# Performance work log

Hardware: AMD Instinct MI355X
Metric: run time of the kernel (lower is better)

The kernel has to match this reference:

```python
import jax, jax.numpy as jnp
import numpy as np

TEMPERATURE = 0.1
EPS = 1e-8


def setup_inputs() -> dict:
    key = jax.random.key(0)
    k1, k2 = jax.random.split(key)
    N, D = 4096, 512
    features = jax.random.normal(k1, (N, D), dtype=jnp.float32)
    labels = jax.random.randint(k2, (N,), 0, 100, dtype=jnp.int64)
    return {"features": features, "labels": labels}


def reference(features, labels):
    # FFT along feature dim -> complex (N, D)
    cf = jnp.fft.fft(features)
    N = cf.shape[0]

    # All-pairs complex dot product expressed as a GEMM:
    # Re(sum_d u_d * conj(v_d)) for every (anchor, contrast) pair -> (N, N)
    dot_real = jnp.real(cf @ jnp.conj(cf).T)

    # L2 norm of complex vectors: sqrt(sum |cf|^2) -> (N,)
    norms = jnp.linalg.norm(cf, axis=-1)

    sim = dot_real / (norms[:, None] * norms[None, :])  # cosine sim (N, N)
    sim = sim / TEMPERATURE

    # Positive-pair mask (same label), excluding the diagonal (self)
    same_label = (labels[:, None] == labels[None, :]).astype(sim.dtype)
    logits_mask = 1.0 - jnp.eye(N, dtype=sim.dtype)
    mask = same_label * logits_mask

    # Faithful to the original: exp without max-subtraction (sim bounded by 1/tau)
    exp_logits = jnp.exp(sim) * logits_mask
    log_prob = sim - jnp.log(exp_logits.sum(axis=1, keepdims=True))

    mean_log_prob_pos = (mask * log_prob).sum(axis=1) / (mask.sum(axis=1) + EPS)
    return -mean_log_prob_pos.mean()
```

## Files before the change

### kernel.cpp

```cpp
#include <hip/hip_runtime.h>
#include <hip/hip_bf16.h>
#include <math.h>


#define NROWS 4096
#define DDIM  512
#define BAND  128
#define NBAND (NROWS / BAND)
#define NPAIR (NBAND * (NBAND + 1) / 2)
#define NSTEP 16

typedef __attribute__((ext_vector_type(4))) float floatx4;

__device__ inline long f8pack(float v0, float v1, float v2, float v3,
                              float v4, float v5, float v6, float v7) {
    int lo = 0, hi = 0;
    lo = __builtin_amdgcn_cvt_pk_fp8_f32(v0, v1, lo, false);
    lo = __builtin_amdgcn_cvt_pk_fp8_f32(v2, v3, lo, true);
    hi = __builtin_amdgcn_cvt_pk_fp8_f32(v4, v5, hi, false);
    hi = __builtin_amdgcn_cvt_pk_fp8_f32(v6, v7, hi, true);
    return ((long)(unsigned)lo) | ((long)hi << 32);
}

__device__ inline float dpp_add16(float v) {
    v += __int_as_float(__builtin_amdgcn_update_dpp(
        0, __float_as_int(v), 0xB1, 0xF, 0xF, true));
    v += __int_as_float(__builtin_amdgcn_update_dpp(
        0, __float_as_int(v), 0x4E, 0xF, 0xF, true));
    v += __int_as_float(__builtin_amdgcn_update_dpp(
        0, __float_as_int(v), 0x141, 0xF, 0xF, true));
    v += __int_as_float(__builtin_amdgcn_update_dpp(
        0, __float_as_int(v), 0x140, 0xF, 0xF, true));
    return v;
}

__global__ __launch_bounds__(256) void prep_kernel(
    const float* __restrict__ F, const int* __restrict__ labels,
    long* __restrict__ Fq, float* __restrict__ invn,
    float* __restrict__ S, float* __restrict__ P, int* __restrict__ hist) {
    const int g = blockIdx.x, t = threadIdx.x;
    const int l = t & 63, w = t >> 6;
    const int row = g * 16 + (l & 15);
    const int koff = ((l >> 4) & 3) * 8;
    float ss = 0.f;
#pragma unroll
    for (int c = 0; c < 4; ++c) {
        const int s = c * 4 + w;
        const int k = s * 32 + koff;
        const float4* src = (const float4*)(F + (size_t)row * DDIM + k);
        float4 a = src[0], b = src[1];
        ss += a.x * a.x + a.y * a.y + a.z * a.z + a.w * a.w
            + b.x * b.x + b.y * b.y + b.z * b.z + b.w * b.w;
        Fq[(size_t)(g * 16 + s) * 64 + l] =
            f8pack(a.x, a.y, a.z, a.w, b.x, b.y, b.z, b.w);
    }
    ss += __shfl_xor(ss, 16, 64);
    ss += __shfl_xor(ss, 32, 64);
    __shared__ float rs[4][16];
    if (l < 16) rs[w][l] = ss;
    __syncthreads();
    if (t < 16) {
        float tot = rs[0][t] + rs[1][t] + rs[2][t] + rs[3][t];
        int r = g * 16 + t;
        invn[r] = rsqrtf(tot) * 3.16227766017f;
        S[r] = 0.f;
        P[r] = 0.f;
    }
    if (g == 0) {
        __shared__ int h[128];
        if (t < 128) h[t] = 0;
        __syncthreads();
        for (int i = t; i < NROWS; i += 256) atomicAdd(&h[labels[i]], 1);
        __syncthreads();
        if (t < 128) hist[t] = h[t];
    }
}

__global__ __launch_bounds__(256) void gemm_kernel(
    const long* __restrict__ Fq, const float* __restrict__ invn,
    const int* __restrict__ labels,
    float* __restrict__ S, float* __restrict__ P) {
    __shared__ long Asl[BAND * 64];

    const int tid = threadIdx.x;
    const int w = tid >> 6, lane = tid & 63;
    const int lrow = lane & 15, lquad = lane >> 4;

    int wid = blockIdx.x;
    int bi = 0;
    while ((bi + 1) * NBAND - (bi + 1) * bi / 2 <= wid) ++bi;
    const int bj = bi + (wid - (bi * NBAND - bi * (bi - 1) / 2));
    const bool diag = (bi == bj);
    const int ib = bi * BAND, jb = bj * BAND;

    {
        const long* src = Fq + (size_t)bi * 8192;
#pragma unroll
        for (int r = 0; r < 16; ++r) {
            __builtin_amdgcn_global_load_lds(
                (const __attribute__((address_space(1))) unsigned int*)
                    (src + r * 512 + (size_t)tid * 2),
                (__attribute__((address_space(3))) unsigned int*)
                    (Asl + r * 512 + tid * 2),
                16, 0, 0);
        }
    }
    __syncthreads();

    floatx4 acc[8][2];
#pragma unroll
    for (int mi = 0; mi < 8; ++mi) {
        acc[mi][0] = (floatx4){0.f, 0.f, 0.f, 0.f};
        acc[mi][1] = (floatx4){0.f, 0.f, 0.f, 0.f};
    }

    const long* pB0 = Fq + (size_t)(bj * 8 + w * 2) * 1024 + lane;
    const long* pB1 = Fq + (size_t)(bj * 8 + w * 2 + 1) * 1024 + lane;

    long bring[2][2];
    bring[0][0] = pB0[0];
    bring[0][1] = pB1[0];
    bring[1][0] = pB0[64];
    bring[1][1] = pB1[64];

#pragma unroll
    for (int ks = 0; ks < NSTEP; ++ks) {
        const int cur = ks & 1;
        const long b0 = bring[cur][0], b1 = bring[cur][1];
        if (ks + 2 < NSTEP) {
            bring[cur][0] = pB0[(ks + 2) * 64];
            bring[cur][1] = pB1[(ks + 2) * 64];
        }
        long a[8];
#pragma unroll
        for (int mi = 0; mi < 8; ++mi)
            a[mi] = Asl[(mi * 16 + ks) * 64 + lane];
#pragma unroll
        for (int mi = 0; mi < 8; ++mi) {
            acc[mi][0] = __builtin_amdgcn_mfma_f32_16x16x32_fp8_fp8(
                a[mi], b0, acc[mi][0], 0, 0, 0);
            acc[mi][1] = __builtin_amdgcn_mfma_f32_16x16x32_fp8_fp8(
                a[mi], b1, acc[mi][1], 0, 0, 0);
        }
    }

    __syncthreads();
    float* er = (float*)Asl;
    float* pr = er + 128;
    float* ec = pr + 128;
    float* pc = ec + 128;
    ((float*)Asl)[tid] = 0.f;
    ((float*)Asl)[tid + 256] = 0.f;
    __syncthreads();

    float inB[2];
    int lB[2];
#pragma unroll
    for (int ni = 0; ni < 2; ++ni) {
        int j = jb + (w * 2 + ni) * 16 + lrow;
        inB[ni] = invn[j];
        lB[ni] = labels[j];
    }

    float ecol[2] = {0.f, 0.f}, pcol[2] = {0.f, 0.f};
#pragma unroll
    for (int mi = 0; mi < 8; ++mi) {
#pragma unroll
        for (int r = 0; r < 4; ++r) {
            const int il = mi * 16 + lquad * 4 + r;
            const int i = ib + il;
            const float inA = invn[i];
            const int lA = labels[i];
            float es = 0.f, ps = 0.f;
#pragma unroll
            for (int ni = 0; ni < 2; ++ni) {
                const int j = jb + (w * 2 + ni) * 16 + lrow;
                float sim = acc[mi][ni][r] * inA * inB[ni];
                float e = __expf(sim);
                float pm = (lA == lB[ni]) ? sim : 0.f;
                if (diag && i == j) { e = 0.f; pm = 0.f; }
                es += e; ps += pm;
                ecol[ni] += e; pcol[ni] += pm;
            }
            es = dpp_add16(es);
            ps = dpp_add16(ps);
            if (lrow == 0) {
                atomicAdd(&er[il], es);
                atomicAdd(&pr[il], ps);
            }
        }
    }
#pragma unroll
    for (int ni = 0; ni < 2; ++ni) {
        float e = ecol[ni], p = pcol[ni];
        e += __shfl_xor(e, 16, 64);
        e += __shfl_xor(e, 32, 64);
        p += __shfl_xor(p, 16, 64);
        p += __shfl_xor(p, 32, 64);
        if (lquad == 0) {
            atomicAdd(&ec[(w * 2 + ni) * 16 + lrow], e);
            atomicAdd(&pc[(w * 2 + ni) * 16 + lrow], p);
        }
    }
    __syncthreads();
    if (tid < 128) {
        atomicAdd(&S[ib + tid], er[tid]);
        atomicAdd(&P[ib + tid], pr[tid]);
    } else if (!diag) {
        atomicAdd(&S[jb + tid - 128], ec[tid - 128]);
        atomicAdd(&P[jb + tid - 128], pc[tid - 128]);
    }
}

__global__ __launch_bounds__(256) void final_kernel(
    const float* __restrict__ S, const float* __restrict__ P,
    const int* __restrict__ labels, const int* __restrict__ hist,
    float* __restrict__ out) {
    float local = 0.f;
    for (int i = threadIdx.x; i < NROWS; i += 256) {
        float cnt = (float)(hist[labels[i]] - 1);
        local += (P[i] - cnt * logf(S[i])) / (cnt + 1e-8f);
    }
#pragma unroll
    for (int m = 1; m < 64; m <<= 1) local += __shfl_xor(local, m, 64);
    __shared__ float red[4];
    int wave = threadIdx.x >> 6;
    if ((threadIdx.x & 63) == 0) red[wave] = local;
    __syncthreads();
    if (threadIdx.x == 0)
        out[0] = -(red[0] + red[1] + red[2] + red[3]) / (float)NROWS;
}

extern "C" void kernel_launch(void* const* d_in, const int* in_sizes, int n_in,
                              void* d_out, int out_size, void* d_ws, size_t ws_size,
                              hipStream_t stream) {
    const float* F = (const float*)d_in[0];
    const int* labels = (const int*)d_in[1];
    float* out = (float*)d_out;

    long* Fq = (long*)d_ws;
    float* invn = (float*)((char*)d_ws + (size_t)NROWS * DDIM);
    float* S = invn + NROWS;
    float* P = S + NROWS;
    int* hist = (int*)(P + NROWS);

    prep_kernel<<<dim3(NROWS / 16), dim3(256), 0, stream>>>(
        F, labels, Fq, invn, S, P, hist);
    gemm_kernel<<<dim3(NPAIR), dim3(256), 0, stream>>>(
        Fq, invn, labels, S, P);
    final_kernel<<<dim3(1), dim3(256), 0, stream>>>(S, P, labels, hist, out);
}
```

Baseline: 95.06 us.

## Fuse prep, GEMM and final reduction into one persistent kernel with grid barriers

Replaces the three separate kernels with a single persistent kernel of 264 workgroups. A spin-wait global barrier on atomic counters separates the quantize/norm phase, the tiled FP8 MFMA pass (each workgroup takes two of the 528 band pairs) and the final reduction done by workgroup 0. The aim is to remove kernel launch gaps and tail effects. It also deepens the B-operand register prefetch from two stages to three. The grid barrier depends on all 264 workgroups being co-resident, and it adds a small init kernel plus spin overhead.

```diff
diff --git a/kernel.cpp b/kernel.cpp
--- a/kernel.cpp
+++ b/kernel.cpp
@@ -8,6 +8,7 @@
 #define BAND  128
 #define NBAND (NROWS / BAND)
 #define NPAIR (NBAND * (NBAND + 1) / 2)
+#define NWG   264
 #define NSTEP 16
 
 typedef __attribute__((ext_vector_type(4))) float floatx4;
@@ -34,201 +35,218 @@
     return v;
 }
 
-__global__ __launch_bounds__(256) void prep_kernel(
+__global__ __launch_bounds__(64) void init_bar(int* __restrict__ bar) {
+    if (threadIdx.x < 8) bar[threadIdx.x] = 0;
+}
+
+__device__ inline void gbar(int* __restrict__ bar, int slot) {
+    __syncthreads();
+    if (threadIdx.x == 0) {
+        __threadfence();
+        atomicAdd(&bar[slot], 1);
+        while (__hip_atomic_load(&bar[slot], __ATOMIC_RELAXED,
+                                 __HIP_MEMORY_SCOPE_AGENT) < NWG)
+            __builtin_amdgcn_s_sleep(2);
+        __threadfence();
+    }
+    __syncthreads();
+}
+
+__global__ __launch_bounds__(256, 2) void fused_all(
     const float* __restrict__ F, const int* __restrict__ labels,
     long* __restrict__ Fq, float* __restrict__ invn,
-    float* __restrict__ S, float* __restrict__ P, int* __restrict__ hist) {
-    const int g = blockIdx.x, t = threadIdx.x;
-    const int l = t & 63, w = t >> 6;
-    const int row = g * 16 + (l & 15);
-    const int koff = ((l >> 4) & 3) * 8;
-    float ss = 0.f;
-#pragma unroll
-    for (int c = 0; c < 4; ++c) {
-        const int s = c * 4 + w;
-        const int k = s * 32 + koff;
-        const float4* src = (const float4*)(F + (size_t)row * DDIM + k);
-        float4 a = src[0], b = src[1];
-        ss += a.x * a.x + a.y * a.y + a.z * a.z + a.w * a.w
-            + b.x * b.x + b.y * b.y + b.z * b.z + b.w * b.w;
-        Fq[(size_t)(g * 16 + s) * 64 + l] =
-            f8pack(a.x, a.y, a.z, a.w, b.x, b.y, b.z, b.w);
-    }
-    ss += __shfl_xor(ss, 16, 64);
-    ss += __shfl_xor(ss, 32, 64);
-    __shared__ float rs[4][16];
-    if (l < 16) rs[w][l] = ss;
-    __syncthreads();
-    if (t < 16) {
-        float tot = rs[0][t] + rs[1][t] + rs[2][t] + rs[3][t];
-        int r = g * 16 + t;
-        invn[r] = rsqrtf(tot) * 3.16227766017f;
-        S[r] = 0.f;
-        P[r] = 0.f;
-    }
-    if (g == 0) {
-        __shared__ int h[128];
-        if (t < 128) h[t] = 0;
-        __syncthreads();
-        for (int i = t; i < NROWS; i += 256) atomicAdd(&h[labels[i]], 1);
-        __syncthreads();
-        if (t < 128) hist[t] = h[t];
-    }
-}
-
-__global__ __launch_bounds__(256) void gemm_kernel(
-    const long* __restrict__ Fq, const float* __restrict__ invn,
-    const int* __restrict__ labels,
-    float* __restrict__ S, float* __restrict__ P) {
+    float* __restrict__ S, float* __restrict__ P,
+    int* __restrict__ hist, int* __restrict__ bar,
+    float* __restrict__ out) {
     __shared__ long Asl[BAND * 64];
-
+    const int wg = blockIdx.x;
     const int tid = threadIdx.x;
     const int w = tid >> 6, lane = tid & 63;
     const int lrow = lane & 15, lquad = lane >> 4;
 
-    int wid = blockIdx.x;
-    int bi = 0;
-    while ((bi + 1) * NBAND - (bi + 1) * bi / 2 <= wid) ++bi;
-    const int bj = bi + (wid - (bi * NBAND - bi * (bi - 1) / 2));
-    const bool diag = (bi == bj);
-    const int ib = bi * BAND, jb = bj * BAND;
-
-    {
-        const long* src = Fq + (size_t)bi * 8192;
-#pragma unroll
-        for (int r = 0; r < 16; ++r) {
-            __builtin_amdgcn_global_load_lds(
-                (const __attribute__((address_space(1))) unsigned int*)
-                    (src + r * 512 + (size_t)tid * 2),
-                (__attribute__((address_space(3))) unsigned int*)
-                    (Asl + r * 512 + tid * 2),
-                16, 0, 0);
-        }
-    }
-    __syncthreads();
-
-    floatx4 acc[8][2];
-#pragma unroll
-    for (int mi = 0; mi < 8; ++mi) {
-        acc[mi][0] = (floatx4){0.f, 0.f, 0.f, 0.f};
-        acc[mi][1] = (floatx4){0.f, 0.f, 0.f, 0.f};
-    }
-
-    const long* pB0 = Fq + (size_t)(bj * 8 + w * 2) * 1024 + lane;
-    const long* pB1 = Fq + (size_t)(bj * 8 + w * 2 + 1) * 1024 + lane;
-
-    long bring[2][2];
-    bring[0][0] = pB0[0];
-    bring[0][1] = pB1[0];
-    bring[1][0] = pB0[64];
-    bring[1][1] = pB1[64];
-
-#pragma unroll
-    for (int ks = 0; ks < NSTEP; ++ks) {
-        const int cur = ks & 1;
-        const long b0 = bring[cur][0], b1 = bring[cur][1];
-        if (ks + 2 < NSTEP) {
-            bring[cur][0] = pB0[(ks + 2) * 64];
-            bring[cur][1] = pB1[(ks + 2) * 64];
-        }
-        long a[8];
-#pragma unroll
-        for (int mi = 0; mi < 8; ++mi)
-            a[mi] = Asl[(mi * 16 + ks) * 64 + lane];
+    if (wg < NROWS / 16) {
+        const int g = wg;
+        const int row = g * 16 + (lane & 15);
+        const int koff = ((lane >> 4) & 3) * 8;
+        float ss = 0.f;
+#pragma unroll
+        for (int c = 0; c < 4; ++c) {
+            const int s = c * 4 + w;
+            const int k = s * 32 + koff;
+            const float4* src = (const float4*)(F + (size_t)row * DDIM + k);
+            float4 a = src[0], b = src[1];
+            ss += a.x * a.x + a.y * a.y + a.z * a.z + a.w * a.w
+                + b.x * b.x + b.y * b.y + b.z * b.z + b.w * b.w;
+            Fq[(size_t)(g * 16 + s) * 64 + lane] =
+                f8pack(a.x, a.y, a.z, a.w, b.x, b.y, b.z, b.w);
+        }
+        ss += __shfl_xor(ss, 16, 64);
+        ss += __shfl_xor(ss, 32, 64);
+        float* rs = (float*)Asl;
+        if (lane < 16) rs[w * 16 + lane] = ss;
+        __syncthreads();
+        if (tid < 16) {
+            float tot = rs[tid] + rs[16 + tid] + rs[32 + tid] + rs[48 + tid];
+            int r = g * 16 + tid;
+            invn[r] = rsqrtf(tot) * 3.16227766017f;
+            S[r] = 0.f;
+            P[r] = 0.f;
+        }
+        if (g == 0) {
+            int* h = (int*)Asl + 64;
+            __syncthreads();
+            if (tid < 128) h[tid] = 0;
+            __syncthreads();
+            for (int i = tid; i < NROWS; i += 256) atomicAdd(&h[labels[i]], 1);
+            __syncthreads();
+            if (tid < 128) hist[tid] = h[tid];
+        }
+    }
+    gbar(bar, 0);
+
+#pragma unroll 1
+    for (int rep = 0; rep < 2; ++rep) {
+        const int wid = wg + rep * NWG;
+        int bi = 0;
+        while ((bi + 1) * NBAND - (bi + 1) * bi / 2 <= wid) ++bi;
+        const int bj = bi + (wid - (bi * NBAND - bi * (bi - 1) / 2));
+        const bool diag = (bi == bj);
+        const int ib = bi * BAND, jb = bj * BAND;
+
+        __syncthreads();
+        {
+            const long* src = Fq + (size_t)bi * 8192;
+#pragma unroll
+            for (int r = 0; r < 16; ++r) {
+                __builtin_amdgcn_global_load_lds(
+                    (const __attribute__((address_space(1))) unsigned int*)
+                        (src + r * 512 + (size_t)tid * 2),
+                    (__attribute__((address_space(3))) unsigned int*)
+                        (Asl + r * 512 + tid * 2),
+                    16, 0, 0);
+            }
+        }
+        __syncthreads();
+
+        floatx4 acc[8][2];
 #pragma unroll
         for (int mi = 0; mi < 8; ++mi) {
-            acc[mi][0] = __builtin_amdgcn_mfma_f32_16x16x32_fp8_fp8(
-                a[mi], b0, acc[mi][0], 0, 0, 0);
-            acc[mi][1] = __builtin_amdgcn_mfma_f32_16x16x32_fp8_fp8(
-                a[mi], b1, acc[mi][1], 0, 0, 0);
-        }
-    }
-
-    __syncthreads();
-    float* er = (float*)Asl;
-    float* pr = er + 128;
-    float* ec = pr + 128;
-    float* pc = ec + 128;
-    ((float*)Asl)[tid] = 0.f;
-    ((float*)Asl)[tid + 256] = 0.f;
-    __syncthreads();
-
-    float inB[2];
-    int lB[2];
-#pragma unroll
-    for (int ni = 0; ni < 2; ++ni) {
-        int j = jb + (w * 2 + ni) * 16 + lrow;
-        inB[ni] = invn[j];
-        lB[ni] = labels[j];
-    }
-
-    float ecol[2] = {0.f, 0.f}, pcol[2] = {0.f, 0.f};
-#pragma unroll
-    for (int mi = 0; mi < 8; ++mi) {
-#pragma unroll
-        for (int r = 0; r < 4; ++r) {
-            const int il = mi * 16 + lquad * 4 + r;
-            const int i = ib + il;
-            const float inA = invn[i];
-            const int lA = labels[i];
-            float es = 0.f, ps = 0.f;
-#pragma unroll
-            for (int ni = 0; ni < 2; ++ni) {
-                const int j = jb + (w * 2 + ni) * 16 + lrow;
-                float sim = acc[mi][ni][r] * inA * inB[ni];
-                float e = __expf(sim);
-                float pm = (lA == lB[ni]) ? sim : 0.f;
-                if (diag && i == j) { e = 0.f; pm = 0.f; }
-                es += e; ps += pm;
-                ecol[ni] += e; pcol[ni] += pm;
-            }
-            es = dpp_add16(es);
-            ps = dpp_add16(ps);
-            if (lrow == 0) {
-                atomicAdd(&er[il], es);
-                atomicAdd(&pr[il], ps);
-            }
-        }
-    }
-#pragma unroll
-    for (int ni = 0; ni < 2; ++ni) {
-        float e = ecol[ni], p = pcol[ni];
-        e += __shfl_xor(e, 16, 64);
-        e += __shfl_xor(e, 32, 64);
-        p += __shfl_xor(p, 16, 64);
-        p += __shfl_xor(p, 32, 64);
-        if (lquad == 0) {
-            atomicAdd(&ec[(w * 2 + ni) * 16 + lrow], e);
-            atomicAdd(&pc[(w * 2 + ni) * 16 + lrow], p);
-        }
-    }
-    __syncthreads();
-    if (tid < 128) {
-        atomicAdd(&S[ib + tid], er[tid]);
-        atomicAdd(&P[ib + tid], pr[tid]);
-    } else if (!diag) {
-        atomicAdd(&S[jb + tid - 128], ec[tid - 128]);
-        atomicAdd(&P[jb + tid - 128], pc[tid - 128]);
-    }
-}
-
-__global__ __launch_bounds__(256) void final_kernel(
-    const float* __restrict__ S, const float* __restrict__ P,
-    const int* __restrict__ labels, const int* __restrict__ hist,
-    float* __restrict__ out) {
-    float local = 0.f;
-    for (int i = threadIdx.x; i < NROWS; i += 256) {
-        float cnt = (float)(hist[labels[i]] - 1);
-        local += (P[i] - cnt * logf(S[i])) / (cnt + 1e-8f);
-    }
-#pragma unroll
-    for (int m = 1; m < 64; m <<= 1) local += __shfl_xor(local, m, 64);
-    __shared__ float red[4];
-    int wave = threadIdx.x >> 6;
-    if ((threadIdx.x & 63) == 0) red[wave] = local;
-    __syncthreads();
-    if (threadIdx.x == 0)
-        out[0] = -(red[0] + red[1] + red[2] + red[3]) / (float)NROWS;
+            acc[mi][0] = (floatx4){0.f, 0.f, 0.f, 0.f};
+            acc[mi][1] = (floatx4){0.f, 0.f, 0.f, 0.f};
+        }
+
+        const long* pB0 = Fq + (size_t)(bj * 8 + w * 2) * 1024 + lane;
+        const long* pB1 = pB0 + 1024;
+        long br0[3], br1[3];
+        br0[0] = pB0[0];   br1[0] = pB1[0];
+        br0[1] = pB0[64];  br1[1] = pB1[64];
+        br0[2] = pB0[128]; br1[2] = pB1[128];
+
+#pragma unroll
+        for (int ks = 0; ks < NSTEP; ++ks) {
+            const int cur = ks % 3;
+            const long b0 = br0[cur], b1 = br1[cur];
+            if (ks + 3 < NSTEP) {
+                br0[cur] = pB0[(ks + 3) * 64];
+                br1[cur] = pB1[(ks + 3) * 64];
+            }
+            long a[8];
+#pragma unroll
+            for (int mi = 0; mi < 8; ++mi)
+                a[mi] = Asl[(mi * 16 + ks) * 64 + lane];
+#pragma unroll
+            for (int mi = 0; mi < 8; ++mi) {
+                acc[mi][0] = __builtin_amdgcn_mfma_f32_16x16x32_fp8_fp8(
+                    a[mi], b0, acc[mi][0], 0, 0, 0);
+                acc[mi][1] = __builtin_amdgcn_mfma_f32_16x16x32_fp8_fp8(
+                    a[mi], b1, acc[mi][1], 0, 0, 0);
+            }
+        }
+
+        __syncthreads();
+        float* er = (float*)Asl;
+        float* pr = er + 128;
+        float* ec = pr + 128;
+        float* pc = ec + 128;
+        ((float*)Asl)[tid] = 0.f;
+        ((float*)Asl)[tid + 256] = 0.f;
+        __syncthreads();
+
+        float inB[2];
+        int lB[2];
+#pragma unroll
+        for (int ni = 0; ni < 2; ++ni) {
+            int j = jb + (w * 2 + ni) * 16 + lrow;
+            inB[ni] = invn[j];
+            lB[ni] = labels[j];
+        }
+
+        float ecol[2] = {0.f, 0.f}, pcol[2] = {0.f, 0.f};
+#pragma unroll
+        for (int mi = 0; mi < 8; ++mi) {
+#pragma unroll
+            for (int r = 0; r < 4; ++r) {
+                const int il = mi * 16 + lquad * 4 + r;
+                const int i = ib + il;
+                const float inA = invn[i];
+                const int lA = labels[i];
+                float es = 0.f, ps = 0.f;
+#pragma unroll
+                for (int ni = 0; ni < 2; ++ni) {
+                    const int j = jb + (w * 2 + ni) * 16 + lrow;
+                    float sim = acc[mi][ni][r] * inA * inB[ni];
+                    float e = __expf(sim);
+                    float pm = (lA == lB[ni]) ? sim : 0.f;
+                    if (diag && i == j) { e = 0.f; pm = 0.f; }
+                    es += e; ps += pm;
+                    ecol[ni] += e; pcol[ni] += pm;
+                }
+                es = dpp_add16(es);
+                ps = dpp_add16(ps);
+                if (lrow == 0) {
+                    atomicAdd(&er[il], es);
+                    atomicAdd(&pr[il], ps);
+                }
+            }
+        }
+#pragma unroll
+        for (int ni = 0; ni < 2; ++ni) {
+            float e = ecol[ni], p = pcol[ni];
+            e += __shfl_xor(e, 16, 64);
+            e += __shfl_xor(e, 32, 64);
+            p += __shfl_xor(p, 16, 64);
+            p += __shfl_xor(p, 32, 64);
+            if (lquad == 0) {
+                atomicAdd(&ec[(w * 2 + ni) * 16 + lrow], e);
+                atomicAdd(&pc[(w * 2 + ni) * 16 + lrow], p);
+            }
+        }
+        __syncthreads();
+        if (tid < 128) {
+            atomicAdd(&S[ib + tid], er[tid]);
+            atomicAdd(&P[ib + tid], pr[tid]);
+        } else if (!diag) {
+            atomicAdd(&S[jb + tid - 128], ec[tid - 128]);
+            atomicAdd(&P[jb + tid - 128], pc[tid - 128]);
+        }
+    }
+    gbar(bar, 1);
+
+    if (wg == 0) {
+        float local = 0.f;
+        for (int i = tid; i < NROWS; i += 256) {
+            float cnt = (float)(hist[labels[i]] - 1);
+            local += (P[i] - cnt * logf(S[i])) / (cnt + 1e-8f);
+        }
+#pragma unroll
+        for (int m = 1; m < 64; m <<= 1) local += __shfl_xor(local, m, 64);
+        float* red = (float*)Asl;
+        __syncthreads();
+        if ((tid & 63) == 0) red[w] = local;
+        __syncthreads();
+        if (tid == 0)
+            out[0] = -(red[0] + red[1] + red[2] + red[3]) / (float)NROWS;
+    }
 }
 
 extern "C" void kernel_launch(void* const* d_in, const int* in_sizes, int n_in,
@@ -243,10 +261,9 @@
     float* S = invn + NROWS;
     float* P = S + NROWS;
     int* hist = (int*)(P + NROWS);
-
-    prep_kernel<<<dim3(NROWS / 16), dim3(256), 0, stream>>>(
-        F, labels, Fq, invn, S, P, hist);
-    gemm_kernel<<<dim3(NPAIR), dim3(256), 0, stream>>>(
-        Fq, invn, labels, S, P);
-    final_kernel<<<dim3(1), dim3(256), 0, stream>>>(S, P, labels, hist, out);
-}
+    int* bar = hist + 128;
+
+    init_bar<<<dim3(1), dim3(64), 0, stream>>>(bar);
+    fused_all<<<dim3(NWG), dim3(256), 0, stream>>>(
+        F, labels, Fq, invn, S, P, hist, bar, out);
+}
```

Result: slower. 131.6 us (+38.4%).

## Replace triangular banded GEMM with full-grid per-wave 64x64 tiles

Applied to the files above, without the earlier changes.

The kernel drops the symmetric upper-triangular 128-row band scheme, which used LDS staging and shared-memory reductions. Each wave now independently computes a 64x64 tile over the full N×N grid, loading A and B operands straight from global memory, and atomically adds its row sums into S and P. This removes the LDS round trips, barriers and the serial triangular index search, and gives much finer parallelism. In exchange it does about twice the MFMA work because symmetry is no longer exploited, issues many more global atomics, and reloads operands per wave.

```diff
diff --git a/kernel.cpp b/kernel.cpp
--- a/kernel.cpp
+++ b/kernel.cpp
@@ -5,9 +5,7 @@
 
 #define NROWS 4096
 #define DDIM  512
-#define BAND  128
-#define NBAND (NROWS / BAND)
-#define NPAIR (NBAND * (NBAND + 1) / 2)
+#define NBG   (NROWS / 64)
 #define NSTEP 16
 
 typedef __attribute__((ext_vector_type(4))) float floatx4;
@@ -76,139 +74,72 @@
     }
 }
 
-__global__ __launch_bounds__(256) void gemm_kernel(
+__global__ __launch_bounds__(256, 4) void gemm_kernel(
     const long* __restrict__ Fq, const float* __restrict__ invn,
     const int* __restrict__ labels,
     float* __restrict__ S, float* __restrict__ P) {
-    __shared__ long Asl[BAND * 64];
+    const int wid = blockIdx.x * 4 + (threadIdx.x >> 6);
+    const int lane = threadIdx.x & 63;
+    const int lrow = lane & 15, lquad = lane >> 4;
+    const int bi = wid >> 6, bj = wid & 63;
 
-    const int tid = threadIdx.x;
-    const int w = tid >> 6, lane = tid & 63;
-    const int lrow = lane & 15, lquad = lane >> 4;
+    const long* pA = Fq + (size_t)(bi * 4) * 1024 + lane;
+    const long* pB = Fq + (size_t)(bj * 4) * 1024 + lane;
 
-    int wid = blockIdx.x;
-    int bi = 0;
-    while ((bi + 1) * NBAND - (bi + 1) * bi / 2 <= wid) ++bi;
-    const int bj = bi + (wid - (bi * NBAND - bi * (bi - 1) / 2));
-    const bool diag = (bi == bj);
-    const int ib = bi * BAND, jb = bj * BAND;
-
-    {
-        const long* src = Fq + (size_t)bi * 8192;
+    floatx4 acc[4][4];
 #pragma unroll
-        for (int r = 0; r < 16; ++r) {
-            __builtin_amdgcn_global_load_lds(
-                (const __attribute__((address_space(1))) unsigned int*)
-                    (src + r * 512 + (size_t)tid * 2),
-                (__attribute__((address_space(3))) unsigned int*)
-                    (Asl + r * 512 + tid * 2),
-                16, 0, 0);
-        }
-    }
-    __syncthreads();
-
-    floatx4 acc[8][2];
+    for (int mi = 0; mi < 4; ++mi)
 #pragma unroll
-    for (int mi = 0; mi < 8; ++mi) {
-        acc[mi][0] = (floatx4){0.f, 0.f, 0.f, 0.f};
-        acc[mi][1] = (floatx4){0.f, 0.f, 0.f, 0.f};
-    }
-
-    const long* pB0 = Fq + (size_t)(bj * 8 + w * 2) * 1024 + lane;
-    const long* pB1 = Fq + (size_t)(bj * 8 + w * 2 + 1) * 1024 + lane;
-
-    long bring[2][2];
-    bring[0][0] = pB0[0];
-    bring[0][1] = pB1[0];
-    bring[1][0] = pB0[64];
-    bring[1][1] = pB1[64];
+        for (int ni = 0; ni < 4; ++ni) acc[mi][ni] = (floatx4){0.f, 0.f, 0.f, 0.f};
 
 #pragma unroll
     for (int ks = 0; ks < NSTEP; ++ks) {
-        const int cur = ks & 1;
-        const long b0 = bring[cur][0], b1 = bring[cur][1];
-        if (ks + 2 < NSTEP) {
-            bring[cur][0] = pB0[(ks + 2) * 64];
-            bring[cur][1] = pB1[(ks + 2) * 64];
-        }
-        long a[8];
+        long av[4], bv[4];
 #pragma unroll
-        for (int mi = 0; mi < 8; ++mi)
-            a[mi] = Asl[(mi * 16 + ks) * 64 + lane];
+        for (int mi = 0; mi < 4; ++mi) av[mi] = pA[mi * 1024 + ks * 64];
 #pragma unroll
-        for (int mi = 0; mi < 8; ++mi) {
-            acc[mi][0] = __builtin_amdgcn_mfma_f32_16x16x32_fp8_fp8(
-                a[mi], b0, acc[mi][0], 0, 0, 0);
-            acc[mi][1] = __builtin_amdgcn_mfma_f32_16x16x32_fp8_fp8(
-                a[mi], b1, acc[mi][1], 0, 0, 0);
-        }
+        for (int ni = 0; ni < 4; ++ni) bv[ni] = pB[ni * 1024 + ks * 64];
+#pragma unroll
+        for (int mi = 0; mi < 4; ++mi)
+#pragma unroll
+            for (int ni = 0; ni < 4; ++ni)
+                acc[mi][ni] = __builtin_amdgcn_mfma_f32_16x16x32_fp8_fp8(
+                    av[mi], bv[ni], acc[mi][ni], 0, 0, 0);
     }
 
-    __syncthreads();
-    float* er = (float*)Asl;
-    float* pr = er + 128;
-    float* ec = pr + 128;
-    float* pc = ec + 128;
-    ((float*)Asl)[tid] = 0.f;
-    ((float*)Asl)[tid + 256] = 0.f;
-    __syncthreads();
-
-    float inB[2];
-    int lB[2];
+    float inB[4];
+    int lB[4];
 #pragma unroll
-    for (int ni = 0; ni < 2; ++ni) {
-        int j = jb + (w * 2 + ni) * 16 + lrow;
+    for (int ni = 0; ni < 4; ++ni) {
+        int j = bj * 64 + ni * 16 + lrow;
         inB[ni] = invn[j];
         lB[ni] = labels[j];
     }
-
-    float ecol[2] = {0.f, 0.f}, pcol[2] = {0.f, 0.f};
 #pragma unroll
-    for (int mi = 0; mi < 8; ++mi) {
+    for (int mi = 0; mi < 4; ++mi) {
 #pragma unroll
         for (int r = 0; r < 4; ++r) {
-            const int il = mi * 16 + lquad * 4 + r;
-            const int i = ib + il;
+            const int i = bi * 64 + mi * 16 + lquad * 4 + r;
             const float inA = invn[i];
             const int lA = labels[i];
             float es = 0.f, ps = 0.f;
 #pragma unroll
-            for (int ni = 0; ni < 2; ++ni) {
-                const int j = jb + (w * 2 + ni) * 16 + lrow;
+            for (int ni = 0; ni < 4; ++ni) {
+                const int j = bj * 64 + ni * 16 + lrow;
                 float sim = acc[mi][ni][r] * inA * inB[ni];
                 float e = __expf(sim);
                 float pm = (lA == lB[ni]) ? sim : 0.f;
-                if (diag && i == j) { e = 0.f; pm = 0.f; }
-                es += e; ps += pm;
-                ecol[ni] += e; pcol[ni] += pm;
+                if (bi == bj && i == j) { e = 0.f; pm = 0.f; }
+                es += e;
+                ps += pm;
             }
             es = dpp_add16(es);
             ps = dpp_add16(ps);
             if (lrow == 0) {
-                atomicAdd(&er[il], es);
-                atomicAdd(&pr[il], ps);
+                atomicAdd(&S[i], es);
+                atomicAdd(&P[i], ps);
             }
         }
-    }
-#pragma unroll
-    for (int ni = 0; ni < 2; ++ni) {
-        float e = ecol[ni], p = pcol[ni];
-        e += __shfl_xor(e, 16, 64);
-        e += __shfl_xor(e, 32, 64);
-        p += __shfl_xor(p, 16, 64);
-        p += __shfl_xor(p, 32, 64);
-        if (lquad == 0) {
-            atomicAdd(&ec[(w * 2 + ni) * 16 + lrow], e);
-            atomicAdd(&pc[(w * 2 + ni) * 16 + lrow], p);
-        }
-    }
-    __syncthreads();
-    if (tid < 128) {
-        atomicAdd(&S[ib + tid], er[tid]);
-        atomicAdd(&P[ib + tid], pr[tid]);
-    } else if (!diag) {
-        atomicAdd(&S[jb + tid - 128], ec[tid - 128]);
-        atomicAdd(&P[jb + tid - 128], pc[tid - 128]);
     }
 }
 
@@ -246,7 +177,7 @@
 
     prep_kernel<<<dim3(NROWS / 16), dim3(256), 0, stream>>>(
         F, labels, Fq, invn, S, P, hist);
-    gemm_kernel<<<dim3(NPAIR), dim3(256), 0, stream>>>(
+    gemm_kernel<<<dim3(NROWS / 64 * NBG / 4), dim3(256), 0, stream>>>(
         Fq, invn, labels, S, P);
     final_kernel<<<dim3(1), dim3(256), 0, stream>>>(S, P, labels, hist, out);
 }
```

Measured after the change: 106.3 us. 1.12x slower.
